# Kernel optimization log

Hardware: AMD Instinct MI355X
Metric: run time of the kernel (lower is better)

Reference implementation:

```python
import jax, jax.numpy as jnp
import numpy as np

N_NODES = 65536
N_EDGES = 524288
N_LAYERS = 3
D = 128
ED = 32
BATCH = 64
NEG_SLOPE = 0.2


def setup_inputs() -> dict:
    key = jax.random.key(0)
    ks = jax.random.split(key, 10)
    w_scale = 1.0 / np.sqrt(D)
    return {
        "x": jax.random.normal(ks[0], (N_NODES, D), dtype=jnp.float32),
        "edge_index": jax.random.randint(ks[1], (2, N_EDGES), 0, N_NODES, dtype=jnp.int32),
        "edge_attr": jax.random.normal(ks[2], (N_EDGES, ED), dtype=jnp.float32),
        "Ws": jax.random.normal(ks[3], (N_LAYERS, D, D), dtype=jnp.float32) * w_scale,
        "att_src": jax.random.normal(ks[4], (N_LAYERS, D), dtype=jnp.float32) * w_scale,
        "att_dst": jax.random.normal(ks[5], (N_LAYERS, D), dtype=jnp.float32) * w_scale,
        "W_edge": jax.random.normal(ks[6], (N_LAYERS, ED, D), dtype=jnp.float32) * (1.0 / np.sqrt(ED)),
        "att_edge": jax.random.normal(ks[7], (N_LAYERS, D), dtype=jnp.float32) * w_scale,
        "bias": jnp.zeros((N_LAYERS, D), dtype=jnp.float32),
        "batch_size": BATCH,
    }


def _gat_layer(x, src, dst, ea, W, a_s, a_d, We, a_e, b, n):
    # PyG GATConv, heads=1, concat=True, flow source_to_target.
    h = x @ W                                      # [N, D]
    al = (h @ a_s)[src] + (h @ a_d)[dst] + (ea @ We) @ a_e   # [E]
    al = jax.nn.leaky_relu(al, NEG_SLOPE)
    # segment softmax over destination-node neighborhoods
    m = jax.ops.segment_max(al, dst, num_segments=n)
    ex = jnp.exp(al - m[dst])
    den = jax.ops.segment_sum(ex, dst, num_segments=n)
    w = ex / den[dst]                              # [E]
    out = jax.ops.segment_sum(w[:, None] * h[src], dst, num_segments=n)
    return out + b


def reference(x, edge_index, edge_attr, Ws, att_src, att_dst, W_edge, att_edge, bias, batch_size):
    n = x.shape[0]
    # add_self_loops with fill_value='mean': self-loop edge_attr is the mean of
    # incoming edge features per destination node (zero if no incoming edges).
    loop = jnp.arange(n, dtype=edge_index.dtype)
    src = jnp.concatenate([edge_index[0], loop])
    dst = jnp.concatenate([edge_index[1], loop])
    cnt = jax.ops.segment_sum(jnp.ones((edge_attr.shape[0],), edge_attr.dtype), edge_index[1], num_segments=n)
    fill = jax.ops.segment_sum(edge_attr, edge_index[1], num_segments=n) / jnp.maximum(cnt, 1.0)[:, None]
    ea = jnp.concatenate([edge_attr, fill], axis=0)

    h = x
    for l in range(Ws.shape[0]):
        h = jax.nn.gelu(
            _gat_layer(h, src, dst, ea, Ws[l], att_src[l], att_dst[l], W_edge[l], att_edge[l], bias[l], n),
            approximate=False,
        )
        # dropout p=0.2 is identity in eval mode
    return h.reshape(batch_size, n // batch_size, -1)
```

## Files before the change

### kernel.cpp

```cpp
#include <hip/hip_runtime.h>
#include <math.h>

#define NN 65536
#define NE 524288
#define D 128
#define ED 32
#define NEG_SLOPE 0.2f

typedef short bf16x8 __attribute__((ext_vector_type(8)));
typedef float f32x4 __attribute__((ext_vector_type(4)));
typedef unsigned short ushort_t;

__device__ __forceinline__ float leaky(float x) { return x > 0.f ? x : NEG_SLOPE * x; }
__device__ __forceinline__ float gelu_exact(float x) {
    return 0.5f * x * (1.f + erff(x * 0.70710678118654752440f));
}
__device__ __forceinline__ unsigned short bf16_rne(float x) {
    unsigned u = __float_as_uint(x);
    return (unsigned short)((u + 0x7FFFu + ((u >> 16) & 1u)) >> 16);
}
__device__ __forceinline__ void unpack8(int4 r, float* f) {
    unsigned u0 = (unsigned)r.x, u1 = (unsigned)r.y, u2 = (unsigned)r.z, u3 = (unsigned)r.w;
    f[0] = __uint_as_float(u0 << 16); f[1] = __uint_as_float(u0 & 0xFFFF0000u);
    f[2] = __uint_as_float(u1 << 16); f[3] = __uint_as_float(u1 & 0xFFFF0000u);
    f[4] = __uint_as_float(u2 << 16); f[5] = __uint_as_float(u2 & 0xFFFF0000u);
    f[6] = __uint_as_float(u3 << 16); f[7] = __uint_as_float(u3 & 0xFFFF0000u);
}


__global__ void k_wvec(const float* __restrict__ We, const float* __restrict__ ae, float* __restrict__ wvec) {
    int t = threadIdx.x;
    if (t < 3 * ED) {
        int l = t / ED, k = t % ED;
        const float* w = We + (long)(l * ED + k) * D;
        const float* a = ae + (long)l * D;
        float s = 0.f;
        #pragma unroll
        for (int i = 0; i < D; ++i) s += w[i] * a[i];
        wvec[t] = s;
    }
}

__global__ void k_ale_hist(const float* __restrict__ ea, const float* __restrict__ wvec,
                           const int* __restrict__ dstArr, int* __restrict__ deg,
                           float* __restrict__ ale0, float* __restrict__ ale1,
                           float* __restrict__ ale2) {
    int e = blockIdx.x * 256 + threadIdx.x;
    atomicAdd(&deg[dstArr[e]], 1);
    const float4* row = (const float4*)(ea + (long)e * ED);
    const float4* w0 = (const float4*)(wvec);
    const float4* w1 = (const float4*)(wvec + ED);
    const float4* w2 = (const float4*)(wvec + 2 * ED);
    float s0 = 0.f, s1 = 0.f, s2 = 0.f;
    #pragma unroll
    for (int i = 0; i < ED / 4; ++i) {
        float4 v = row[i];
        float4 a = w0[i], b = w1[i], c = w2[i];
        s0 += v.x * a.x + v.y * a.y + v.z * a.z + v.w * a.w;
        s1 += v.x * b.x + v.y * b.y + v.z * b.z + v.w * b.w;
        s2 += v.x * c.x + v.y * c.y + v.z * c.z + v.w * c.w;
    }
    ale0[e] = s0;
    ale1[e] = s1;
    ale2[e] = s2;
}

__global__ void k_scan1(const int* __restrict__ deg, int* __restrict__ rp, int* __restrict__ bsum) {
    __shared__ int s[256];
    int t = threadIdx.x;
    int i = blockIdx.x * 256 + t;
    int v = deg[i];
    s[t] = v;
    __syncthreads();
    #pragma unroll
    for (int off = 1; off < 256; off <<= 1) {
        int x = (t >= off) ? s[t - off] : 0;
        __syncthreads();
        s[t] += x;
        __syncthreads();
    }
    rp[i] = s[t] - v;
    if (t == 255) bsum[blockIdx.x] = s[t];
}

__global__ void k_scan2(const int* __restrict__ bsum, int* __restrict__ bscan, int* __restrict__ rp) {
    __shared__ int s[256];
    int t = threadIdx.x;
    int v = bsum[t];
    s[t] = v;
    __syncthreads();
    #pragma unroll
    for (int off = 1; off < 256; off <<= 1) {
        int x = (t >= off) ? s[t - off] : 0;
        __syncthreads();
        s[t] += x;
        __syncthreads();
    }
    bscan[t] = s[t] - v;
    if (t == 255) rp[NN] = s[t];
}

__global__ void k_scan3(int* __restrict__ rp, const int* __restrict__ bscan, int* __restrict__ cursor) {
    int i = blockIdx.x * 256 + threadIdx.x;
    int v = rp[i] + bscan[blockIdx.x];
    rp[i] = v;
    cursor[i] = v;
}

__global__ void k_scatter4(const int* __restrict__ srcArr, const int* __restrict__ dstArr,
                           int* __restrict__ cursor, const float* __restrict__ ale0,
                           const float* __restrict__ ale1, const float* __restrict__ ale2,
                           int4* __restrict__ edata) {
    int base = blockIdx.x * 1024 + threadIdx.x;
    int e[4], d[4], p[4];
    #pragma unroll
    for (int i = 0; i < 4; ++i) e[i] = base + 256 * i;
    #pragma unroll
    for (int i = 0; i < 4; ++i) d[i] = dstArr[e[i]];
    #pragma unroll
    for (int i = 0; i < 4; ++i) p[i] = atomicAdd(&cursor[d[i]], 1);
    #pragma unroll
    for (int i = 0; i < 4; ++i) {
        edata[p[i]] = make_int4(srcArr[e[i]], __float_as_int(ale0[e[i]]),
                                __float_as_int(ale1[e[i]]), __float_as_int(ale2[e[i]]));
    }
}

__global__ void k_wpack(const float* __restrict__ Ws, short* __restrict__ Whp, short* __restrict__ Wlp) {
    int t = blockIdx.x * 256 + threadIdx.x;
    if (t >= 3 * 4 * 4 * 128) return;
    int n = t & 127;
    int q = (t >> 7) & 3;
    int ks = (t >> 9) & 3;
    int l = t >> 11;
    const float* w = Ws + (size_t)l * D * D;
    size_t obase = (size_t)l * D * D + ((size_t)((ks * 4 + q) * 128) + n) * 8;
    #pragma unroll
    for (int j = 0; j < 8; ++j) {
        float x = w[(size_t)(ks * 32 + q * 8 + j) * D + n];
        unsigned short hb = bf16_rne(x);
        float hf = __uint_as_float(((unsigned)hb) << 16);
        Whp[obase + j] = (short)hb;
        Wlp[obase + j] = (short)bf16_rne(x - hf);
    }
}


__global__ __launch_bounds__(256) void k_gemm_mfma(const float* __restrict__ A,
        const short* __restrict__ Whp, const short* __restrict__ Wlp,
        const float* __restrict__ a_s, const float* __restrict__ a_d,
        ushort_t* __restrict__ Hb, float* __restrict__ als, float* __restrict__ ald) {
    __shared__ int4 Bs[2048];
    int t = threadIdx.x;
    int wave = t >> 6, lane = t & 63;
    int l16 = lane & 15, q = lane >> 4;
    int rows_base = blockIdx.x * 128 + wave * 32;

    const int4* wh4 = (const int4*)Whp;
    const int4* wl4 = (const int4*)Wlp;
    const short* bsh = (const short*)Bs;
    const short* bsl = (const short*)(Bs + 1024);

    f32x4 acc[2][8] = {};
    #pragma unroll
    for (int h2 = 0; h2 < 2; ++h2) {
        if (h2) __syncthreads();
        #pragma unroll
        for (int i = 0; i < 4; ++i) {
            Bs[t + 256 * i] = wh4[h2 * 1024 + t + 256 * i];
            Bs[1024 + t + 256 * i] = wl4[h2 * 1024 + t + 256 * i];
        }
        __syncthreads();
        #pragma unroll
        for (int kk = 0; kk < 2; ++kk) {
            int ks = h2 * 2 + kk;
            bf16x8 ah[2], alo[2];
            #pragma unroll
            for (int mt = 0; mt < 2; ++mt) {
                const float* ap = A + (size_t)(rows_base + mt * 16 + l16) * D + ks * 32 + q * 8;
                float4 v0 = *(const float4*)ap;
                float4 v1 = *(const float4*)(ap + 4);
                float f[8] = {v0.x, v0.y, v0.z, v0.w, v1.x, v1.y, v1.z, v1.w};
                #pragma unroll
                for (int j = 0; j < 8; ++j) {
                    unsigned short hb = bf16_rne(f[j]);
                    float hf = __uint_as_float(((unsigned)hb) << 16);
                    ah[mt][j]  = (short)hb;
                    alo[mt][j] = (short)bf16_rne(f[j] - hf);
                }
            }
            #pragma unroll
            for (int nt = 0; nt < 8; ++nt) {
                int idx = (((kk * 4 + q) * 128) + nt * 16 + l16) * 8;
                bf16x8 bh = *(const bf16x8*)(bsh + idx);
                bf16x8 bl = *(const bf16x8*)(bsl + idx);
                #pragma unroll
                for (int mt = 0; mt < 2; ++mt) {
                    acc[mt][nt] = __builtin_amdgcn_mfma_f32_16x16x32_bf16(bh, ah[mt], acc[mt][nt], 0, 0, 0);
                    acc[mt][nt] = __builtin_amdgcn_mfma_f32_16x16x32_bf16(bl, ah[mt], acc[mt][nt], 0, 0, 0);
                    acc[mt][nt] = __builtin_amdgcn_mfma_f32_16x16x32_bf16(bh, alo[mt], acc[mt][nt], 0, 0, 0);
                }
            }
        }
    }


    float av[8][4], dv[8][4];
    #pragma unroll
    for (int nt = 0; nt < 8; ++nt) {
        float4 a4 = *(const float4*)(a_s + nt * 16 + q * 4);
        float4 d4 = *(const float4*)(a_d + nt * 16 + q * 4);
        av[nt][0] = a4.x; av[nt][1] = a4.y; av[nt][2] = a4.z; av[nt][3] = a4.w;
        dv[nt][0] = d4.x; dv[nt][1] = d4.y; dv[nt][2] = d4.z; dv[nt][3] = d4.w;
    }
    #pragma unroll
    for (int mt = 0; mt < 2; ++mt) {
        float ps = 0.f, pd = 0.f;
        #pragma unroll
        for (int nt = 0; nt < 8; ++nt) {
            #pragma unroll
            for (int r = 0; r < 4; ++r) {
                float v = acc[mt][nt][r];
                ps += v * av[nt][r];
                pd += v * dv[nt][r];
            }
        }
        ps += __shfl_xor(ps, 16); pd += __shfl_xor(pd, 16);
        ps += __shfl_xor(ps, 32); pd += __shfl_xor(pd, 32);
        if (q == 0) {
            als[rows_base + mt * 16 + l16] = ps;
            ald[rows_base + mt * 16 + l16] = pd;
        }
    }

    __syncthreads();
    char* tb = (char*)Bs + wave * 8192;
    #pragma unroll
    for (int mt = 0; mt < 2; ++mt) {
        int row = mt * 16 + l16;
        unsigned key = (unsigned)(row & 7) << 4;
        #pragma unroll
        for (int nt = 0; nt < 8; ++nt) {
            ushort4 pk;
            pk.x = bf16_rne(acc[mt][nt][0]);
            pk.y = bf16_rne(acc[mt][nt][1]);
            pk.z = bf16_rne(acc[mt][nt][2]);
            pk.w = bf16_rne(acc[mt][nt][3]);
            unsigned byteoff = (unsigned)row * 256u + (unsigned)(nt * 16 + q * 4) * 2u;
            *(ushort4*)(tb + (byteoff ^ key)) = pk;
        }
    }
    __syncthreads();
    #pragma unroll
    for (int i = 0; i < 8; ++i) {
        int m = lane + 64 * i;
        unsigned row = (unsigned)m >> 4;
        unsigned byteoff = (unsigned)m * 16u;
        unsigned addr = byteoff ^ ((row & 7u) << 4);
        int4 v = *(const int4*)(tb + addr);
        *(int4*)((char*)Hb + (size_t)rows_base * 256 + (size_t)m * 16) = v;
    }
}

__global__ __launch_bounds__(256) void k_aggr_fused(const ushort_t* __restrict__ hb,
        const float* __restrict__ als, const float* __restrict__ ald,
        const int4* __restrict__ edata, const int* __restrict__ rp,
        const float* __restrict__ bias, int lsel, float* __restrict__ out_f32) {
    int t = threadIdx.x;
    int lane = t & 63;
    int l16 = lane & 15;
    int qb = lane & 48;
    int n = blockIdx.x * 16 + (t >> 4);
    int s = rp[n], e = rp[n + 1];
    int deg = e - s;
    float aldd = ald[n];
    float alsn = als[n];
    float inv_deg = (deg > 0) ? 1.f / (float)deg : 0.f;

    int4 hvp = *(const int4*)(hb + (size_t)n * D + l16 * 8);
    float acc8[8];

    if (deg <= 16) {
        int sn0 = 0;
        float al0 = -1e30f, alev0 = 0.f;
        if (l16 < deg) {
            int4 ed = edata[s + l16];
            sn0 = ed.x;
            alev0 = __int_as_float((lsel == 0) ? ed.y : ((lsel == 1) ? ed.z : ed.w));
            al0 = leaky(als[sn0] + aldd + alev0);
        }
        float mm = al0, asum = alev0;
        #pragma unroll
        for (int off = 1; off < 16; off <<= 1) {
            mm = fmaxf(mm, __shfl_xor(mm, off));
            asum += __shfl_xor(asum, off);
        }
        float self_al = leaky(alsn + aldd + asum * inv_deg);
        mm = fmaxf(mm, self_al);
        float p0 = (l16 < deg) ? __expf(al0 - mm) : 0.f;
        float den = p0;
        #pragma unroll
        for (int off = 1; off < 16; off <<= 1) den += __shfl_xor(den, off);
        float es = __expf(self_al - mm);
        den += es;
        float inv = 1.f / den;
        float w0 = p0 * inv;
        float wself = es * inv;

        float fv[8];
        unpack8(hvp, fv);
        #pragma unroll
        for (int j = 0; j < 8; ++j) acc8[j] = wself * fv[j];

        int tt = 0;
        for (; tt + 4 <= deg; tt += 4) {
            int   sA = __shfl(sn0, qb + tt),     sB = __shfl(sn0, qb + tt + 1);
            int   sC = __shfl(sn0, qb + tt + 2), sD = __shfl(sn0, qb + tt + 3);
            float wA = __shfl(w0, qb + tt),      wB = __shfl(w0, qb + tt + 1);
            float wC = __shfl(w0, qb + tt + 2),  wD = __shfl(w0, qb + tt + 3);
            int4 rA = *(const int4*)(hb + (size_t)sA * D + l16 * 8);
            int4 rB = *(const int4*)(hb + (size_t)sB * D + l16 * 8);
            int4 rC = *(const int4*)(hb + (size_t)sC * D + l16 * 8);
            int4 rD = *(const int4*)(hb + (size_t)sD * D + l16 * 8);
            float fA[8], fB[8], fC[8], fD[8];
            unpack8(rA, fA); unpack8(rB, fB); unpack8(rC, fC); unpack8(rD, fD);
            #pragma unroll
            for (int j = 0; j < 8; ++j)
                acc8[j] += wA * fA[j] + wB * fB[j] + wC * fC[j] + wD * fD[j];
        }
        for (; tt < deg; ++tt) {
            int st = __shfl(sn0, qb + tt);
            float wt = __shfl(w0, qb + tt);
            int4 r = *(const int4*)(hb + (size_t)st * D + l16 * 8);
            float f[8];
            unpack8(r, f);
            #pragma unroll
            for (int j = 0; j < 8; ++j) acc8[j] += wt * f[j];
        }
    } else {
        float mm = -1e30f, asum = 0.f;
        for (int base = s; base < e; base += 16) {
            int j = base + l16;
            if (j < e) {
                int4 ed = edata[j];
                float alev = __int_as_float((lsel == 0) ? ed.y : ((lsel == 1) ? ed.z : ed.w));
                asum += alev;
                mm = fmaxf(mm, leaky(als[ed.x] + aldd + alev));
            }
        }
        #pragma unroll
        for (int off = 1; off < 16; off <<= 1) {
            mm = fmaxf(mm, __shfl_xor(mm, off));
            asum += __shfl_xor(asum, off);
        }
        float self_al = leaky(alsn + aldd + asum * inv_deg);
        mm = fmaxf(mm, self_al);
        float den = 0.f;
        for (int base = s; base < e; base += 16) {
            int j = base + l16;
            if (j < e) {
                int4 ed = edata[j];
                float alev = __int_as_float((lsel == 0) ? ed.y : ((lsel == 1) ? ed.z : ed.w));
                den += __expf(leaky(als[ed.x] + aldd + alev) - mm);
            }
        }
        #pragma unroll
        for (int off = 1; off < 16; off <<= 1) den += __shfl_xor(den, off);
        float es = __expf(self_al - mm);
        den += es;
        float inv = 1.f / den;
        float wself = es * inv;
        float fv[8];
        unpack8(hvp, fv);
        #pragma unroll
        for (int j = 0; j < 8; ++j) acc8[j] = wself * fv[j];
        for (int base = s; base < e; base += 16) {
            int cnt = min(e - base, 16);
            int sn = 0;
            float w = 0.f;
            if (l16 < cnt) {
                int4 ed = edata[base + l16];
                sn = ed.x;
                float alev = __int_as_float((lsel == 0) ? ed.y : ((lsel == 1) ? ed.z : ed.w));
                w = __expf(leaky(als[sn] + aldd + alev) - mm) * inv;
            }
            for (int tt = 0; tt < cnt; ++tt) {
                int st = __shfl(sn, qb + tt);
                float wt = __shfl(w, qb + tt);
                int4 r = *(const int4*)(hb + (size_t)st * D + l16 * 8);
                float f[8];
                unpack8(r, f);
                #pragma unroll
                for (int j = 0; j < 8; ++j) acc8[j] += wt * f[j];
            }
        }
    }

    const float4* b4 = (const float4*)(bias + l16 * 8);
    float4 b0 = b4[0], b1 = b4[1];
    float bb[8] = {b0.x, b0.y, b0.z, b0.w, b1.x, b1.y, b1.z, b1.w};
    float o[8];
    #pragma unroll
    for (int j = 0; j < 8; ++j) o[j] = gelu_exact(acc8[j] + bb[j]);

    float4* o4 = (float4*)(out_f32 + (size_t)n * D + l16 * 8);
    o4[0] = make_float4(o[0], o[1], o[2], o[3]);
    o4[1] = make_float4(o[4], o[5], o[6], o[7]);
}


extern "C" void kernel_launch(void* const* d_in, const int* in_sizes, int n_in,
                              void* d_out, int out_size, void* d_ws, size_t ws_size,
                              hipStream_t stream) {
    (void)in_sizes; (void)n_in; (void)out_size; (void)ws_size;
    const float* x        = (const float*)d_in[0];
    const int*   eidx     = (const int*)d_in[1];
    const float* ea       = (const float*)d_in[2];
    const float* Ws       = (const float*)d_in[3];
    const float* att_src  = (const float*)d_in[4];
    const float* att_dst  = (const float*)d_in[5];
    const float* W_edge   = (const float*)d_in[6];
    const float* att_edge = (const float*)d_in[7];
    const float* bias     = (const float*)d_in[8];
    float* out = (float*)d_out;

    char* ws = (char*)d_ws;
    size_t off = 0;
    auto alloc = [&](size_t bytes) {
        void* p = ws + off;
        off += (bytes + 255) & ~(size_t)255;
        return p;
    };
    ushort_t* Hb   = (ushort_t*)alloc((size_t)NN * D * 2);
    float*    Hx   = (float*)alloc((size_t)NN * D * 4);
    float*    als  = (float*)alloc((size_t)NN * 4);
    float*    ald  = (float*)alloc((size_t)NN * 4);
    int4*     edata= (int4*)alloc((size_t)NE * 16);
    float*    ale0 = (float*)alloc((size_t)NE * 4);
    float*    ale1 = (float*)alloc((size_t)NE * 4);
    float*    ale2 = (float*)alloc((size_t)NE * 4);
    float*    wvec = (float*)alloc(3 * ED * 4);
    int*      deg  = (int*)alloc((size_t)NN * 4);
    int*      rp   = (int*)alloc((size_t)(NN + 4) * 4);
    int*      cursor = (int*)alloc((size_t)NN * 4);
    int*      bsum = (int*)alloc(256 * 4);
    int*      bscan= (int*)alloc(256 * 4);
    short*    Whp  = (short*)alloc((size_t)3 * D * D * 2);
    short*    Wlp  = (short*)alloc((size_t)3 * D * D * 2);

    const int* e_src = eidx;
    const int* e_dst = eidx + NE;

    hipMemsetAsync(deg, 0, (size_t)NN * 4, stream);
    k_wvec<<<1, 128, 0, stream>>>(W_edge, att_edge, wvec);
    k_ale_hist<<<NE / 256, 256, 0, stream>>>(ea, wvec, e_dst, deg, ale0, ale1, ale2);
    k_scan1<<<NN / 256, 256, 0, stream>>>(deg, rp, bsum);
    k_scan2<<<1, 256, 0, stream>>>(bsum, bscan, rp);
    k_scan3<<<NN / 256, 256, 0, stream>>>(rp, bscan, cursor);
    k_scatter4<<<NE / 1024, 256, 0, stream>>>(e_src, e_dst, cursor, ale0, ale1, ale2, edata);

    k_wpack<<<24, 256, 0, stream>>>(Ws, Whp, Wlp);

    for (int l = 0; l < 3; ++l) {
        k_gemm_mfma<<<NN / 128, 256, 0, stream>>>(l == 0 ? x : Hx,
                                                  Whp + (size_t)l * D * D, Wlp + (size_t)l * D * D,
                                                  att_src + (size_t)l * D, att_dst + (size_t)l * D,
                                                  Hb, als, ald);
        bool last = (l == 2);
        k_aggr_fused<<<NN / 16, 256, 0, stream>>>(Hb, als, ald, edata, rp, bias + (size_t)l * D, l,
                                                  last ? out : Hx);
    }
}
```

Measured before the change: 352.2 us.

## Merge preprocessing kernels, halve GEMM tile, and unroll aggregation gathers

Folds the edge-weight vector, edge-logit/histogram and weight-packing kernels into a single front kernel. The three-pass scan becomes two, and the edge scatter shares a launch with the layer-0 GEMM. The GEMM tile drops from 128 to 64 rows per block to double the block count. The aggregation fast path now issues 8 or 16 neighbour gathers up front instead of a 4-way loop with a remainder. The goal is fewer launches and more memory-level parallelism, at the cost of redundant wvec computation in every block and an aggregation path that now assumes a fixed maximum degree.

```diff
diff --git a/kernel.cpp b/kernel.cpp
--- a/kernel.cpp
+++ b/kernel.cpp
@@ -28,29 +28,51 @@
 }
 
 
-__global__ void k_wvec(const float* __restrict__ We, const float* __restrict__ ae, float* __restrict__ wvec) {
+__global__ __launch_bounds__(256) void k_front(const float* __restrict__ ea,
+        const int* __restrict__ dstArr, int* __restrict__ deg,
+        const float* __restrict__ We, const float* __restrict__ ae,
+        const float* __restrict__ Ws, short* __restrict__ Whp, short* __restrict__ Wlp,
+        float* __restrict__ ale0, float* __restrict__ ale1, float* __restrict__ ale2) {
+    if (blockIdx.x >= NE / 256) {
+        int t = (blockIdx.x - NE / 256) * 256 + threadIdx.x;
+        if (t >= 3 * 4 * 4 * 128) return;
+        int n = t & 127;
+        int q = (t >> 7) & 3;
+        int ks = (t >> 9) & 3;
+        int l = t >> 11;
+        const float* w = Ws + (size_t)l * D * D;
+        size_t obase = (size_t)l * D * D + ((size_t)((ks * 4 + q) * 128) + n) * 8;
+        #pragma unroll
+        for (int j = 0; j < 8; ++j) {
+            float x = w[(size_t)(ks * 32 + q * 8 + j) * D + n];
+            unsigned short hb = bf16_rne(x);
+            float hf = __uint_as_float(((unsigned)hb) << 16);
+            Whp[obase + j] = (short)hb;
+            Wlp[obase + j] = (short)bf16_rne(x - hf);
+        }
+        return;
+    }
+    __shared__ __align__(16) float wv[3 * ED];
     int t = threadIdx.x;
     if (t < 3 * ED) {
-        int l = t / ED, k = t % ED;
-        const float* w = We + (long)(l * ED + k) * D;
-        const float* a = ae + (long)l * D;
+        int l = t >> 5, k = t & 31;
+        const float4* w = (const float4*)(We + (size_t)(l * ED + k) * D);
+        const float4* a = (const float4*)(ae + (size_t)l * D);
         float s = 0.f;
         #pragma unroll
-        for (int i = 0; i < D; ++i) s += w[i] * a[i];
-        wvec[t] = s;
-    }
-}
-
-__global__ void k_ale_hist(const float* __restrict__ ea, const float* __restrict__ wvec,
-                           const int* __restrict__ dstArr, int* __restrict__ deg,
-                           float* __restrict__ ale0, float* __restrict__ ale1,
-                           float* __restrict__ ale2) {
-    int e = blockIdx.x * 256 + threadIdx.x;
+        for (int i = 0; i < D / 4; ++i) {
+            float4 x = w[i], y = a[i];
+            s += x.x * y.x + x.y * y.y + x.z * y.z + x.w * y.w;
+        }
+        wv[t] = s;
+    }
+    __syncthreads();
+    int e = blockIdx.x * 256 + t;
     atomicAdd(&deg[dstArr[e]], 1);
-    const float4* row = (const float4*)(ea + (long)e * ED);
-    const float4* w0 = (const float4*)(wvec);
-    const float4* w1 = (const float4*)(wvec + ED);
-    const float4* w2 = (const float4*)(wvec + 2 * ED);
+    const float4* row = (const float4*)(ea + (size_t)e * ED);
+    const float4* w0 = (const float4*)(wv);
+    const float4* w1 = (const float4*)(wv + ED);
+    const float4* w2 = (const float4*)(wv + 2 * ED);
     float s0 = 0.f, s1 = 0.f, s2 = 0.f;
     #pragma unroll
     for (int i = 0; i < ED / 4; ++i) {
@@ -64,6 +86,7 @@
     ale1[e] = s1;
     ale2[e] = s2;
 }
+
 
 __global__ void k_scan1(const int* __restrict__ deg, int* __restrict__ rp, int* __restrict__ bsum) {
     __shared__ int s[256];
@@ -83,9 +106,10 @@
     if (t == 255) bsum[blockIdx.x] = s[t];
 }
 
-__global__ void k_scan2(const int* __restrict__ bsum, int* __restrict__ bscan, int* __restrict__ rp) {
+__global__ void k_scanF(int* __restrict__ rp, const int* __restrict__ bsum, int* __restrict__ cursor) {
     __shared__ int s[256];
     int t = threadIdx.x;
+    int bid = blockIdx.x;
     int v = bsum[t];
     s[t] = v;
     __syncthreads();
@@ -96,57 +120,16 @@
         s[t] += x;
         __syncthreads();
     }
-    bscan[t] = s[t] - v;
-    if (t == 255) rp[NN] = s[t];
-}
-
-__global__ void k_scan3(int* __restrict__ rp, const int* __restrict__ bscan, int* __restrict__ cursor) {
-    int i = blockIdx.x * 256 + threadIdx.x;
-    int v = rp[i] + bscan[blockIdx.x];
-    rp[i] = v;
-    cursor[i] = v;
-}
-
-__global__ void k_scatter4(const int* __restrict__ srcArr, const int* __restrict__ dstArr,
-                           int* __restrict__ cursor, const float* __restrict__ ale0,
-                           const float* __restrict__ ale1, const float* __restrict__ ale2,
-                           int4* __restrict__ edata) {
-    int base = blockIdx.x * 1024 + threadIdx.x;
-    int e[4], d[4], p[4];
-    #pragma unroll
-    for (int i = 0; i < 4; ++i) e[i] = base + 256 * i;
-    #pragma unroll
-    for (int i = 0; i < 4; ++i) d[i] = dstArr[e[i]];
-    #pragma unroll
-    for (int i = 0; i < 4; ++i) p[i] = atomicAdd(&cursor[d[i]], 1);
-    #pragma unroll
-    for (int i = 0; i < 4; ++i) {
-        edata[p[i]] = make_int4(srcArr[e[i]], __float_as_int(ale0[e[i]]),
-                                __float_as_int(ale1[e[i]]), __float_as_int(ale2[e[i]]));
-    }
-}
-
-__global__ void k_wpack(const float* __restrict__ Ws, short* __restrict__ Whp, short* __restrict__ Wlp) {
-    int t = blockIdx.x * 256 + threadIdx.x;
-    if (t >= 3 * 4 * 4 * 128) return;
-    int n = t & 127;
-    int q = (t >> 7) & 3;
-    int ks = (t >> 9) & 3;
-    int l = t >> 11;
-    const float* w = Ws + (size_t)l * D * D;
-    size_t obase = (size_t)l * D * D + ((size_t)((ks * 4 + q) * 128) + n) * 8;
-    #pragma unroll
-    for (int j = 0; j < 8; ++j) {
-        float x = w[(size_t)(ks * 32 + q * 8 + j) * D + n];
-        unsigned short hb = bf16_rne(x);
-        float hf = __uint_as_float(((unsigned)hb) << 16);
-        Whp[obase + j] = (short)hb;
-        Wlp[obase + j] = (short)bf16_rne(x - hf);
-    }
-}
-
-
-__global__ __launch_bounds__(256) void k_gemm_mfma(const float* __restrict__ A,
+    int add = (bid > 0) ? s[bid - 1] : 0;
+    int i = bid * 256 + t;
+    int r = rp[i] + add;
+    rp[i] = r;
+    cursor[i] = r;
+    if (bid == 255 && t == 255) rp[NN] = NE;
+}
+
+
+__device__ __forceinline__ void gemm_body(int b, const float* __restrict__ A,
         const short* __restrict__ Whp, const short* __restrict__ Wlp,
         const float* __restrict__ a_s, const float* __restrict__ a_d,
         ushort_t* __restrict__ Hb, float* __restrict__ als, float* __restrict__ ald) {
@@ -154,14 +137,14 @@
     int t = threadIdx.x;
     int wave = t >> 6, lane = t & 63;
     int l16 = lane & 15, q = lane >> 4;
-    int rows_base = blockIdx.x * 128 + wave * 32;
+    int rows_base = b * 64 + wave * 16;
 
     const int4* wh4 = (const int4*)Whp;
     const int4* wl4 = (const int4*)Wlp;
     const short* bsh = (const short*)Bs;
     const short* bsl = (const short*)(Bs + 1024);
 
-    f32x4 acc[2][8] = {};
+    f32x4 acc[8] = {};
     #pragma unroll
     for (int h2 = 0; h2 < 2; ++h2) {
         if (h2) __syncthreads();
@@ -174,85 +157,64 @@
         #pragma unroll
         for (int kk = 0; kk < 2; ++kk) {
             int ks = h2 * 2 + kk;
-            bf16x8 ah[2], alo[2];
+            const float* ap = A + (size_t)(rows_base + l16) * D + ks * 32 + q * 8;
+            float4 v0 = *(const float4*)ap;
+            float4 v1 = *(const float4*)(ap + 4);
+            float f[8] = {v0.x, v0.y, v0.z, v0.w, v1.x, v1.y, v1.z, v1.w};
+            bf16x8 ah, alo;
             #pragma unroll
-            for (int mt = 0; mt < 2; ++mt) {
-                const float* ap = A + (size_t)(rows_base + mt * 16 + l16) * D + ks * 32 + q * 8;
-                float4 v0 = *(const float4*)ap;
-                float4 v1 = *(const float4*)(ap + 4);
-                float f[8] = {v0.x, v0.y, v0.z, v0.w, v1.x, v1.y, v1.z, v1.w};
-                #pragma unroll
-                for (int j = 0; j < 8; ++j) {
-                    unsigned short hb = bf16_rne(f[j]);
-                    float hf = __uint_as_float(((unsigned)hb) << 16);
-                    ah[mt][j]  = (short)hb;
-                    alo[mt][j] = (short)bf16_rne(f[j] - hf);
-                }
+            for (int j = 0; j < 8; ++j) {
+                unsigned short hb = bf16_rne(f[j]);
+                float hf = __uint_as_float(((unsigned)hb) << 16);
+                ah[j]  = (short)hb;
+                alo[j] = (short)bf16_rne(f[j] - hf);
             }
             #pragma unroll
             for (int nt = 0; nt < 8; ++nt) {
                 int idx = (((kk * 4 + q) * 128) + nt * 16 + l16) * 8;
                 bf16x8 bh = *(const bf16x8*)(bsh + idx);
                 bf16x8 bl = *(const bf16x8*)(bsl + idx);
-                #pragma unroll
-                for (int mt = 0; mt < 2; ++mt) {
-                    acc[mt][nt] = __builtin_amdgcn_mfma_f32_16x16x32_bf16(bh, ah[mt], acc[mt][nt], 0, 0, 0);
-                    acc[mt][nt] = __builtin_amdgcn_mfma_f32_16x16x32_bf16(bl, ah[mt], acc[mt][nt], 0, 0, 0);
-                    acc[mt][nt] = __builtin_amdgcn_mfma_f32_16x16x32_bf16(bh, alo[mt], acc[mt][nt], 0, 0, 0);
-                }
-            }
-        }
-    }
-
-
-    float av[8][4], dv[8][4];
+                acc[nt] = __builtin_amdgcn_mfma_f32_16x16x32_bf16(bh, ah, acc[nt], 0, 0, 0);
+                acc[nt] = __builtin_amdgcn_mfma_f32_16x16x32_bf16(bl, ah, acc[nt], 0, 0, 0);
+                acc[nt] = __builtin_amdgcn_mfma_f32_16x16x32_bf16(bh, alo, acc[nt], 0, 0, 0);
+            }
+        }
+    }
+
+    float ps = 0.f, pd = 0.f;
     #pragma unroll
     for (int nt = 0; nt < 8; ++nt) {
         float4 a4 = *(const float4*)(a_s + nt * 16 + q * 4);
         float4 d4 = *(const float4*)(a_d + nt * 16 + q * 4);
-        av[nt][0] = a4.x; av[nt][1] = a4.y; av[nt][2] = a4.z; av[nt][3] = a4.w;
-        dv[nt][0] = d4.x; dv[nt][1] = d4.y; dv[nt][2] = d4.z; dv[nt][3] = d4.w;
-    }
-    #pragma unroll
-    for (int mt = 0; mt < 2; ++mt) {
-        float ps = 0.f, pd = 0.f;
-        #pragma unroll
-        for (int nt = 0; nt < 8; ++nt) {
-            #pragma unroll
-            for (int r = 0; r < 4; ++r) {
-                float v = acc[mt][nt][r];
-                ps += v * av[nt][r];
-                pd += v * dv[nt][r];
-            }
-        }
-        ps += __shfl_xor(ps, 16); pd += __shfl_xor(pd, 16);
-        ps += __shfl_xor(ps, 32); pd += __shfl_xor(pd, 32);
-        if (q == 0) {
-            als[rows_base + mt * 16 + l16] = ps;
-            ald[rows_base + mt * 16 + l16] = pd;
-        }
+        ps += acc[nt][0] * a4.x + acc[nt][1] * a4.y + acc[nt][2] * a4.z + acc[nt][3] * a4.w;
+        pd += acc[nt][0] * d4.x + acc[nt][1] * d4.y + acc[nt][2] * d4.z + acc[nt][3] * d4.w;
+    }
+    ps += __shfl_xor(ps, 16); pd += __shfl_xor(pd, 16);
+    ps += __shfl_xor(ps, 32); pd += __shfl_xor(pd, 32);
+    if (q == 0) {
+        als[rows_base + l16] = ps;
+        ald[rows_base + l16] = pd;
     }
 
     __syncthreads();
-    char* tb = (char*)Bs + wave * 8192;
-    #pragma unroll
-    for (int mt = 0; mt < 2; ++mt) {
-        int row = mt * 16 + l16;
+    char* tb = (char*)Bs + wave * 4096;
+    {
+        int row = l16;
         unsigned key = (unsigned)(row & 7) << 4;
         #pragma unroll
         for (int nt = 0; nt < 8; ++nt) {
             ushort4 pk;
-            pk.x = bf16_rne(acc[mt][nt][0]);
-            pk.y = bf16_rne(acc[mt][nt][1]);
-            pk.z = bf16_rne(acc[mt][nt][2]);
-            pk.w = bf16_rne(acc[mt][nt][3]);
+            pk.x = bf16_rne(acc[nt][0]);
+            pk.y = bf16_rne(acc[nt][1]);
+            pk.z = bf16_rne(acc[nt][2]);
+            pk.w = bf16_rne(acc[nt][3]);
             unsigned byteoff = (unsigned)row * 256u + (unsigned)(nt * 16 + q * 4) * 2u;
             *(ushort4*)(tb + (byteoff ^ key)) = pk;
         }
     }
     __syncthreads();
     #pragma unroll
-    for (int i = 0; i < 8; ++i) {
+    for (int i = 0; i < 4; ++i) {
         int m = lane + 64 * i;
         unsigned row = (unsigned)m >> 4;
         unsigned byteoff = (unsigned)m * 16u;
@@ -261,6 +223,42 @@
         *(int4*)((char*)Hb + (size_t)rows_base * 256 + (size_t)m * 16) = v;
     }
 }
+
+__global__ __launch_bounds__(256) void k_scatgemm(
+        const int* __restrict__ srcArr, const int* __restrict__ dstArr,
+        int* __restrict__ cursor, const float* __restrict__ ale0,
+        const float* __restrict__ ale1, const float* __restrict__ ale2,
+        int4* __restrict__ edata,
+        const float* __restrict__ A, const short* __restrict__ Whp,
+        const short* __restrict__ Wlp, const float* __restrict__ a_s,
+        const float* __restrict__ a_d, ushort_t* __restrict__ Hb,
+        float* __restrict__ als, float* __restrict__ ald) {
+    if (blockIdx.x < 256) {
+        int base = blockIdx.x * 2048 + threadIdx.x;
+        int e[8], d[8], p[8];
+        #pragma unroll
+        for (int i = 0; i < 8; ++i) e[i] = base + 256 * i;
+        #pragma unroll
+        for (int i = 0; i < 8; ++i) d[i] = dstArr[e[i]];
+        #pragma unroll
+        for (int i = 0; i < 8; ++i) p[i] = atomicAdd(&cursor[d[i]], 1);
+        #pragma unroll
+        for (int i = 0; i < 8; ++i) {
+            edata[p[i]] = make_int4(srcArr[e[i]], __float_as_int(ale0[e[i]]),
+                                    __float_as_int(ale1[e[i]]), __float_as_int(ale2[e[i]]));
+        }
+        return;
+    }
+    gemm_body(blockIdx.x - 256, A, Whp, Wlp, a_s, a_d, Hb, als, ald);
+}
+
+__global__ __launch_bounds__(256) void k_gemm(const float* __restrict__ A,
+        const short* __restrict__ Whp, const short* __restrict__ Wlp,
+        const float* __restrict__ a_s, const float* __restrict__ a_d,
+        ushort_t* __restrict__ Hb, float* __restrict__ als, float* __restrict__ ald) {
+    gemm_body(blockIdx.x, A, Whp, Wlp, a_s, a_d, Hb, als, ald);
+}
+
 
 __global__ __launch_bounds__(256) void k_aggr_fused(const ushort_t* __restrict__ hb,
         const float* __restrict__ als, const float* __restrict__ ald,
@@ -312,30 +310,36 @@
         #pragma unroll
         for (int j = 0; j < 8; ++j) acc8[j] = wself * fv[j];
 
-        int tt = 0;
-        for (; tt + 4 <= deg; tt += 4) {
-            int   sA = __shfl(sn0, qb + tt),     sB = __shfl(sn0, qb + tt + 1);
-            int   sC = __shfl(sn0, qb + tt + 2), sD = __shfl(sn0, qb + tt + 3);
-            float wA = __shfl(w0, qb + tt),      wB = __shfl(w0, qb + tt + 1);
-            float wC = __shfl(w0, qb + tt + 2),  wD = __shfl(w0, qb + tt + 3);
-            int4 rA = *(const int4*)(hb + (size_t)sA * D + l16 * 8);
-            int4 rB = *(const int4*)(hb + (size_t)sB * D + l16 * 8);
-            int4 rC = *(const int4*)(hb + (size_t)sC * D + l16 * 8);
-            int4 rD = *(const int4*)(hb + (size_t)sD * D + l16 * 8);
-            float fA[8], fB[8], fC[8], fD[8];
-            unpack8(rA, fA); unpack8(rB, fB); unpack8(rC, fC); unpack8(rD, fD);
+        int sA[8]; float wA[8]; int4 rb[8];
+        #pragma unroll
+        for (int i = 0; i < 8; ++i) { sA[i] = __shfl(sn0, qb + i); wA[i] = __shfl(w0, qb + i); }
+        #pragma unroll
+        for (int i = 0; i < 8; ++i) rb[i] = *(const int4*)(hb + (size_t)sA[i] * D + l16 * 8);
+
+        int sB[8]; float wB[8]; int4 rb2[8];
+        #pragma unroll
+        for (int i = 0; i < 8; ++i) { sB[i] = __shfl(sn0, qb + 8 + i); wB[i] = __shfl(w0, qb + 8 + i); }
+        bool more = (deg > 8);
+        if (more) {
             #pragma unroll
-            for (int j = 0; j < 8; ++j)
-                acc8[j] += wA * fA[j] + wB * fB[j] + wC * fC[j] + wD * fD[j];
-        }
-        for (; tt < deg; ++tt) {
-            int st = __shfl(sn0, qb + tt);
-            float wt = __shfl(w0, qb + tt);
-            int4 r = *(const int4*)(hb + (size_t)st * D + l16 * 8);
+            for (int i = 0; i < 8; ++i) rb2[i] = *(const int4*)(hb + (size_t)sB[i] * D + l16 * 8);
+        }
+
+        #pragma unroll
+        for (int i = 0; i < 8; ++i) {
             float f[8];
-            unpack8(r, f);
+            unpack8(rb[i], f);
             #pragma unroll
-            for (int j = 0; j < 8; ++j) acc8[j] += wt * f[j];
+            for (int j = 0; j < 8; ++j) acc8[j] += wA[i] * f[j];
+        }
+        if (more) {
+            #pragma unroll
+            for (int i = 0; i < 8; ++i) {
+                float f[8];
+                unpack8(rb2[i], f);
+                #pragma unroll
+                for (int j = 0; j < 8; ++j) acc8[j] += wB[i] * f[j];
+            }
         }
     } else {
         float mm = -1e30f, asum = 0.f;
@@ -439,12 +443,10 @@
     float*    ale0 = (float*)alloc((size_t)NE * 4);
     float*    ale1 = (float*)alloc((size_t)NE * 4);
     float*    ale2 = (float*)alloc((size_t)NE * 4);
-    float*    wvec = (float*)alloc(3 * ED * 4);
     int*      deg  = (int*)alloc((size_t)NN * 4);
     int*      rp   = (int*)alloc((size_t)(NN + 4) * 4);
     int*      cursor = (int*)alloc((size_t)NN * 4);
     int*      bsum = (int*)alloc(256 * 4);
-    int*      bscan= (int*)alloc(256 * 4);
     short*    Whp  = (short*)alloc((size_t)3 * D * D * 2);
     short*    Wlp  = (short*)alloc((size_t)3 * D * D * 2);
 
@@ -452,20 +454,20 @@
     const int* e_dst = eidx + NE;
 
     hipMemsetAsync(deg, 0, (size_t)NN * 4, stream);
-    k_wvec<<<1, 128, 0, stream>>>(W_edge, att_edge, wvec);
-    k_ale_hist<<<NE / 256, 256, 0, stream>>>(ea, wvec, e_dst, deg, ale0, ale1, ale2);
+    k_front<<<NE / 256 + 24, 256, 0, stream>>>(ea, e_dst, deg, W_edge, att_edge,
+                                               Ws, Whp, Wlp, ale0, ale1, ale2);
     k_scan1<<<NN / 256, 256, 0, stream>>>(deg, rp, bsum);
-    k_scan2<<<1, 256, 0, stream>>>(bsum, bscan, rp);
-    k_scan3<<<NN / 256, 256, 0, stream>>>(rp, bscan, cursor);
-    k_scatter4<<<NE / 1024, 256, 0, stream>>>(e_src, e_dst, cursor, ale0, ale1, ale2, edata);
-
-    k_wpack<<<24, 256, 0, stream>>>(Ws, Whp, Wlp);
+    k_scanF<<<NN / 256, 256, 0, stream>>>(rp, bsum, cursor);
+
+    k_scatgemm<<<256 + NN / 64, 256, 0, stream>>>(e_src, e_dst, cursor, ale0, ale1, ale2, edata,
+                                                  x, Whp, Wlp, att_src, att_dst, Hb, als, ald);
 
     for (int l = 0; l < 3; ++l) {
-        k_gemm_mfma<<<NN / 128, 256, 0, stream>>>(l == 0 ? x : Hx,
-                                                  Whp + (size_t)l * D * D, Wlp + (size_t)l * D * D,
-                                                  att_src + (size_t)l * D, att_dst + (size_t)l * D,
-                                                  Hb, als, ald);
+        if (l > 0) {
+            k_gemm<<<NN / 64, 256, 0, stream>>>(Hx, Whp + (size_t)l * D * D, Wlp + (size_t)l * D * D,
+                                                att_src + (size_t)l * D, att_dst + (size_t)l * D,
+                                                Hb, als, ald);
+        }
         bool last = (l == 2);
         k_aggr_fused<<<NN / 16, 256, 0, stream>>>(Hb, als, ald, edata, rp, bias + (size_t)l * D, l,
                                                   last ? out : Hx);
```

Measured after the change: 351.1 us. Within noise of the previous version (-0.3%).
